# Kernel optimization log

Hardware: AMD Instinct MI355X
Metric: run time of the kernel (lower is better)

The kernel has to match this reference:

```python
import math
import jax, jax.numpy as jnp
import numpy as np

D_MODEL = 1024
NUM_HEADS = 16
HEAD_DIM = D_MODEL // NUM_HEADS
EPS = 1e-8


def setup_inputs() -> dict:
    key = jax.random.key(0)
    ks = jax.random.split(key, 9)
    B, T = 2, 2048
    scale = 1.0 / math.sqrt(D_MODEL)
    return {
        "query": jax.random.normal(ks[0], (B, T, D_MODEL), jnp.float32),
        "key": jax.random.normal(ks[1], (B, T, D_MODEL), jnp.float32),
        "value": jax.random.normal(ks[2], (B, T, D_MODEL), jnp.float32),
        "key_padding_mask": jnp.zeros((B, T), dtype=bool),
        "Wq": jax.random.normal(ks[3], (D_MODEL, D_MODEL), jnp.float32) * scale,
        "Wk": jax.random.normal(ks[4], (D_MODEL, D_MODEL), jnp.float32) * scale,
        "Wv": jax.random.normal(ks[5], (D_MODEL, D_MODEL), jnp.float32) * scale,
        "Wo": jax.random.normal(ks[6], (D_MODEL, D_MODEL), jnp.float32) * scale,
        "s_v": jnp.zeros((NUM_HEADS,), jnp.float32),
        "s_r": jnp.zeros((NUM_HEADS,), jnp.float32),
    }


def _l2norm(x, eps=EPS):
    n = jnp.sqrt(jnp.sum(x * x, axis=-1, keepdims=True))
    return x / jnp.maximum(n, eps)


def _tanh_norm(x, eps=EPS):
    # Reconstructed TanhNorm: bound each head vector by tanh of its L2 norm.
    n = jnp.sqrt(jnp.sum(x * x, axis=-1, keepdims=True))
    return jnp.tanh(n) * x / (n + eps)


def reference(query, key, value, key_padding_mask, Wq, Wk, Wv, Wo, s_v, s_r):
    B, T_q, _ = query.shape
    T_k = key.shape[1]
    H, D = NUM_HEADS, HEAD_DIM

    def proj_split(x, W):  # torch Linear: x @ W.T, then split heads -> (B,H,T,D)
        y = jnp.einsum('btm,dm->btd', x, W)
        return y.reshape(x.shape[0], x.shape[1], H, D).transpose(0, 2, 1, 3)

    q = _l2norm(proj_split(query, Wq))
    k = _l2norm(proj_split(key, Wk))
    v = _l2norm(proj_split(value, Wv))

    sim = jnp.einsum('bhqd,bhkd->bhqk', q, k)  # cosine similarities

    w = jnp.exp(s_v) + 1.0  # (H,) window size per head
    r = jnp.exp(s_r) + 1.0  # (H,) sharpness per head

    # Trim-and-Square: alpha = relu(1 - r*(1 - sim))^2
    alpha = jax.nn.relu(1.0 - r[None, :, None, None] * (1.0 - sim)) ** 2

    # Causal cosine softmask: (H, T_q, T_k)
    rel = (jnp.arange(T_k)[None, :] - jnp.arange(T_q)[:, None]).astype(jnp.float32)
    w_ = w[:, None, None]
    cos_mask = 0.5 * (jnp.cos(jnp.pi * rel[None] / w_) + 1.0)
    in_window = (rel[None] > -w_) & (rel[None] <= 0)
    softmask = cos_mask * in_window.astype(jnp.float32)
    alpha = alpha * softmask[None]

    alpha = jnp.where(key_padding_mask[:, None, None, :], 0.0, alpha)

    out = jnp.einsum('bhqk,bhkd->bhqd', alpha, v)
    out = _tanh_norm(out)
    out = out.transpose(0, 2, 1, 3).reshape(B, T_q, H * D)
    return jnp.einsum('btm,dm->btd', out, Wo)
```

## Files before the change

### kernel.cpp

```cpp
#include <hip/hip_runtime.h>
#include <math.h>

#define D_MODEL 1024
#define NUM_HEADS 16
#define HEAD_DIM 64
#define EPS 1e-8f
#define B_SZ 2
#define T_SZ 2048
#define KEXP 2048

typedef unsigned short ushort_t;
typedef __attribute__((ext_vector_type(8))) short bf16x8;
typedef __attribute__((ext_vector_type(4))) float f32x4;

__device__ __forceinline__ ushort_t f2bf(float f) {
    unsigned u = __float_as_uint(f);
    unsigned r = (u + 0x7FFFu + ((u >> 16) & 1u)) >> 16;
    return (ushort_t)r;
}
__device__ __forceinline__ float bf2f(ushort_t h) {
    return __uint_as_float(((unsigned)h) << 16);
}

__device__ __forceinline__ void gload_lds16(const ushort_t* g, ushort_t* l) {
    __builtin_amdgcn_global_load_lds(
        (const __attribute__((address_space(1))) unsigned int*)g,
        (__attribute__((address_space(3))) unsigned int*)l, 16, 0, 0);
}

__global__ __launch_bounds__(256) void expand7(
    const float* q, const float* k, const float* v,
    const float* wq, const float* wk, const float* wv, const float* wo,
    ushort_t* qe, ushort_t* ke, ushort_t* ve,
    ushort_t* wqe, ushort_t* wke, ushort_t* wve, ushort_t* woe)
{
    const float* in; ushort_t* out; int rows;
    switch (blockIdx.z) {
        case 0: in = q;  out = qe;  rows = 4096; break;
        case 1: in = k;  out = ke;  rows = 4096; break;
        case 2: in = v;  out = ve;  rows = 4096; break;
        case 3: in = wq; out = wqe; rows = 1024; break;
        case 4: in = wk; out = wke; rows = 1024; break;
        case 5: in = wv; out = wve; rows = 1024; break;
        default: in = wo; out = woe; rows = 1024; break;
    }
    const int gid = blockIdx.x * 256 + threadIdx.x;
    const int e = gid * 8;
    if (e >= rows * 1024) return;
    const int row = e >> 10;
    const int kk = e & 1023;

    float x[8];
    *(float4*)&x[0] = *(const float4*)&in[(size_t)row * 1024 + kk];
    *(float4*)&x[4] = *(const float4*)&in[(size_t)row * 1024 + kk + 4];

    union { ushort_t s[8]; uint4 u; } hi, lo;
    #pragma unroll
    for (int i = 0; i < 8; ++i) {
        ushort_t h = f2bf(x[i]);
        hi.s[i] = h;
        lo.s[i] = f2bf(x[i] - bf2f(h));
    }
    ushort_t* dst = out + (size_t)row * KEXP + (kk >> 5) * 64 + (kk & 31);
    *(uint4*)dst        = hi.u;
    *(uint4*)(dst + 32) = lo.u;
}

template<int BN, int WAVES_M, int WAVES_N>
__global__ __launch_bounds__(256) void gemm_split(
    const ushort_t* A0, const ushort_t* B0, float* C0,
    const ushort_t* A1, const ushort_t* B1, float* C1,
    const ushort_t* A2, const ushort_t* B2, float* C2,
    int M, int N)
{
    constexpr int BM = 128;
    constexpr int WAVE_M = BM / WAVES_M;
    constexpr int WAVE_N = BN / WAVES_N;
    constexpr int FM = WAVE_M / 16;
    constexpr int FN = WAVE_N / 16;
    constexpr int NLD = BM / 32 + BN / 32;

    const int gx = gridDim.x, gy = gridDim.y;
    const int nwg = gx * gy * gridDim.z;
    const int lid = blockIdx.x + gx * (blockIdx.y + gy * blockIdx.z);
    const int cpx = nwg >> 3;
    const int swz = (lid & 7) * cpx + (lid >> 3);
    const int bz  = swz / (gx * gy);
    const int rem = swz - bz * gx * gy;
    const int by  = rem / gx;
    const int bx  = rem - by * gx;

    const ushort_t* Ae; const ushort_t* Be; float* C;
    if (bz == 0)      { Ae = A0; Be = B0; C = C0; }
    else if (bz == 1) { Ae = A1; Be = B1; C = C1; }
    else              { Ae = A2; Be = B2; C = C2; }

    __shared__ __align__(16) ushort_t As0[BM * 64];
    __shared__ __align__(16) ushort_t As1[BM * 64];
    __shared__ __align__(16) ushort_t Bs0[BN * 64];
    __shared__ __align__(16) ushort_t Bs1[BN * 64];

    const int tid = threadIdx.x;
    const int bm = by * BM;
    const int bn = bx * BN;

    const int rr = tid >> 3;
    const int p  = tid & 7;

    const int wid  = tid >> 6;
    const int wm   = wid / WAVES_N;
    const int wn   = wid % WAVES_N;
    const int lane = tid & 63;
    const int lrow = lane & 15;
    const int lk   = lane >> 4;

    f32x4 acc[FM][FN] = {};

    auto stage = [&](ushort_t* AsP, ushort_t* BsP, int ks) {
        const int kb = ks * 64;
        #pragma unroll
        for (int r = 0; r < BM / 32; ++r) {
            const int row = r * 32 + rr;
            const int s = p ^ (row & 7);
            gload_lds16(Ae + (size_t)(bm + row) * KEXP + kb + s * 8,
                        &AsP[row * 64 + p * 8]);
        }
        #pragma unroll
        for (int r = 0; r < BN / 32; ++r) {
            const int row = r * 32 + rr;
            const int s = p ^ (row & 7);
            gload_lds16(Be + (size_t)(bn + row) * KEXP + kb + s * 8,
                        &BsP[row * 64 + p * 8]);
        }
    };

    auto compute = [&](const ushort_t* AsP, const ushort_t* BsP) {
        bf16x8 ah[FM], al[FM], bh[FN], bl[FN];
        #pragma unroll
        for (int m = 0; m < FM; ++m) {
            const int row = wm * WAVE_M + m * 16 + lrow;
            const int x = row & 7;
            ah[m] = *(const bf16x8*)&AsP[row * 64 + ((lk)     ^ x) * 8];
            al[m] = *(const bf16x8*)&AsP[row * 64 + ((lk + 4) ^ x) * 8];
        }
        #pragma unroll
        for (int n = 0; n < FN; ++n) {
            const int row = wn * WAVE_N + n * 16 + lrow;
            const int x = row & 7;
            bh[n] = *(const bf16x8*)&BsP[row * 64 + ((lk)     ^ x) * 8];
            bl[n] = *(const bf16x8*)&BsP[row * 64 + ((lk + 4) ^ x) * 8];
        }
        #pragma unroll
        for (int m = 0; m < FM; ++m)
            #pragma unroll
            for (int n = 0; n < FN; ++n) {
                acc[m][n] = __builtin_amdgcn_mfma_f32_16x16x32_bf16(ah[m], bh[n], acc[m][n], 0, 0, 0);
                acc[m][n] = __builtin_amdgcn_mfma_f32_16x16x32_bf16(al[m], bh[n], acc[m][n], 0, 0, 0);
                acc[m][n] = __builtin_amdgcn_mfma_f32_16x16x32_bf16(ah[m], bl[n], acc[m][n], 0, 0, 0);
            }
    };

    auto wait_nld = [&]() {
        if constexpr (NLD == 8)      asm volatile("s_waitcnt vmcnt(8)" ::: "memory");
        else if constexpr (NLD == 6) asm volatile("s_waitcnt vmcnt(6)" ::: "memory");
        else                         asm volatile("s_waitcnt vmcnt(0)" ::: "memory");
    };

    stage(As0, Bs0, 0);

    #pragma unroll 1
    for (int ks = 0; ks < 30; ks += 2) {
        stage(As1, Bs1, ks + 1);
        wait_nld();
        __builtin_amdgcn_s_barrier();
        __builtin_amdgcn_sched_barrier(0);
        compute(As0, Bs0);
        __builtin_amdgcn_s_barrier();

        stage(As0, Bs0, ks + 2);
        wait_nld();
        __builtin_amdgcn_s_barrier();
        __builtin_amdgcn_sched_barrier(0);
        compute(As1, Bs1);
        __builtin_amdgcn_s_barrier();
    }
    stage(As1, Bs1, 31);
    wait_nld();
    __builtin_amdgcn_s_barrier();
    __builtin_amdgcn_sched_barrier(0);
    compute(As0, Bs0);
    __builtin_amdgcn_s_barrier();

    asm volatile("s_waitcnt vmcnt(0)" ::: "memory");
    __builtin_amdgcn_s_barrier();
    __builtin_amdgcn_sched_barrier(0);
    compute(As1, Bs1);

    #pragma unroll
    for (int m = 0; m < FM; ++m)
        #pragma unroll
        for (int j = 0; j < 4; ++j) {
            const int row = bm + wm * WAVE_M + m * 16 + lk * 4 + j;
            float* cr = C + (size_t)row * N + bn + wn * WAVE_N + lrow;
            #pragma unroll
            for (int n = 0; n < FN; ++n)
                cr[n * 16] = acc[m][n][j];
        }
}

__device__ __forceinline__ float wred(float x) {
    #pragma unroll
    for (int off = 32; off; off >>= 1) x += __shfl_xor(x, off);
    return x;
}

__global__ __launch_bounds__(256) void attn_kernel(
    const float* __restrict__ Q, const float* __restrict__ Kp, const float* __restrict__ Vp,
    const int* __restrict__ mask, const float* __restrict__ s_v, const float* __restrict__ s_r,
    ushort_t* __restrict__ Oe)
{
    const int lane = threadIdx.x & 63;
    const int wq = (blockIdx.x * blockDim.x + threadIdx.x) >> 6;
    const int i = wq % T_SZ;
    const int h = (wq / T_SZ) % NUM_HEADS;
    const int b = wq / (T_SZ * NUM_HEADS);

    const float w = expf(s_v[h]) + 1.0f;
    const float r = expf(s_r[h]) + 1.0f;

    const size_t base = (size_t)(b * T_SZ) * D_MODEL + h * HEAD_DIM + lane;

    const float qv = Q[base + (size_t)i * D_MODEL];
    const float qn = qv / fmaxf(sqrtf(wred(qv * qv)), EPS);

    int jmin = i - (int)ceilf(w) + 1;
    if (jmin < 0) jmin = 0;

    float acc = 0.0f;
    for (int j = jmin; j <= i; ++j) {
        const float rel = (float)(j - i);
        if (!(rel > -w)) continue;
        const float kv = Kp[base + (size_t)j * D_MODEL];
        const float kn = kv / fmaxf(sqrtf(wred(kv * kv)), EPS);
        const float sim = wred(qn * kn);
        const float cm = 0.5f * (cosf((float)M_PI * rel / w) + 1.0f);
        const float a1 = fmaxf(1.0f - r * (1.0f - sim), 0.0f);
        float alpha = a1 * a1 * cm;
        if (mask[b * T_SZ + j] != 0) alpha = 0.0f;
        const float vv = Vp[base + (size_t)j * D_MODEL];
        const float vn = vv / fmaxf(sqrtf(wred(vv * vv)), EPS);
        acc += alpha * vn;
    }

    const float n = sqrtf(wred(acc * acc));
    const float o = tanhf(n) * acc / (n + EPS);

    const int row = b * T_SZ + i;
    const int kg  = h * HEAD_DIM + lane;
    ushort_t hi = f2bf(o);
    ushort_t lo = f2bf(o - bf2f(hi));
    ushort_t* dst = Oe + (size_t)row * KEXP + (kg >> 5) * 64 + (kg & 31);
    dst[0]  = hi;
    dst[32] = lo;
}

extern "C" void kernel_launch(void* const* d_in, const int* in_sizes, int n_in,
                              void* d_out, int out_size, void* d_ws, size_t ws_size,
                              hipStream_t stream) {
    const float* query = (const float*)d_in[0];
    const float* key   = (const float*)d_in[1];
    const float* value = (const float*)d_in[2];
    const int*   mask  = (const int*)d_in[3];
    const float* Wq    = (const float*)d_in[4];
    const float* Wk    = (const float*)d_in[5];
    const float* Wv    = (const float*)d_in[6];
    const float* Wo    = (const float*)d_in[7];
    const float* s_v   = (const float*)d_in[8];
    const float* s_r   = (const float*)d_in[9];
    float* out = (float*)d_out;

    const int M = B_SZ * T_SZ;
    const size_t MB = 1u << 20;

    char* ws = (char*)d_ws;
    ushort_t* qe  = (ushort_t*)(ws + 0 * MB);
    ushort_t* ke  = (ushort_t*)(ws + 16 * MB);
    ushort_t* ve  = (ushort_t*)(ws + 32 * MB);
    ushort_t* wqe = (ushort_t*)(ws + 48 * MB);
    ushort_t* wke = (ushort_t*)(ws + 52 * MB);
    ushort_t* wve = (ushort_t*)(ws + 56 * MB);
    ushort_t* woe = (ushort_t*)(ws + 60 * MB);
    float*    qp  = (float*)(ws + 64 * MB);
    float*    kp  = (float*)(ws + 80 * MB);
    float*    vp  = (float*)(ws + 96 * MB);
    ushort_t* aoe = qe;

    hipLaunchKernelGGL(expand7, dim3(2048, 1, 7), dim3(256), 0, stream,
                       query, key, value, Wq, Wk, Wv, Wo,
                       qe, ke, ve, wqe, wke, wve, woe);

    hipLaunchKernelGGL((gemm_split<128, 2, 2>), dim3(D_MODEL / 128, M / 128, 3), dim3(256), 0, stream,
                       qe, wqe, qp,
                       ke, wke, kp,
                       ve, wve, vp,
                       M, D_MODEL);

    const int total_waves = B_SZ * NUM_HEADS * T_SZ;
    hipLaunchKernelGGL(attn_kernel, dim3(total_waves / 4), dim3(256), 0, stream,
                       qp, kp, vp, mask, s_v, s_r, aoe);

    hipLaunchKernelGGL((gemm_split<64, 4, 1>), dim3(D_MODEL / 64, M / 128, 1), dim3(256), 0, stream,
                       aoe, woe, out,
                       aoe, woe, out,
                       aoe, woe, out,
                       M, D_MODEL);
}
```

Baseline: 164.0 us.

## Fuse activation bf16 hi/lo split into QKV projection GEMM

The expand kernel now converts only the four weight matrices. The Q/K/V projection GEMM reads fp32 activations directly, splits them into bf16 hi/lo parts in registers and writes them into swizzled LDS. This removes the write and re-read of the expanded activation buffers (about 48 MB of traffic). The trade-off is that the new GEMM uses single-buffered LDS with synchronous global loads of A and per-iteration conversion work, so it loses the double-buffered pipelining of the old GEMM.

```diff
diff --git a/kernel.cpp b/kernel.cpp
--- a/kernel.cpp
+++ b/kernel.cpp
@@ -28,25 +28,19 @@
         (__attribute__((address_space(3))) unsigned int*)l, 16, 0, 0);
 }
 
-__global__ __launch_bounds__(256) void expand7(
-    const float* q, const float* k, const float* v,
+__global__ __launch_bounds__(256) void expand4(
     const float* wq, const float* wk, const float* wv, const float* wo,
-    ushort_t* qe, ushort_t* ke, ushort_t* ve,
     ushort_t* wqe, ushort_t* wke, ushort_t* wve, ushort_t* woe)
 {
-    const float* in; ushort_t* out; int rows;
+    const float* in; ushort_t* out;
     switch (blockIdx.z) {
-        case 0: in = q;  out = qe;  rows = 4096; break;
-        case 1: in = k;  out = ke;  rows = 4096; break;
-        case 2: in = v;  out = ve;  rows = 4096; break;
-        case 3: in = wq; out = wqe; rows = 1024; break;
-        case 4: in = wk; out = wke; rows = 1024; break;
-        case 5: in = wv; out = wve; rows = 1024; break;
-        default: in = wo; out = woe; rows = 1024; break;
+        case 0: in = wq; out = wqe; break;
+        case 1: in = wk; out = wke; break;
+        case 2: in = wv; out = wve; break;
+        default: in = wo; out = woe; break;
     }
     const int gid = blockIdx.x * 256 + threadIdx.x;
     const int e = gid * 8;
-    if (e >= rows * 1024) return;
     const int row = e >> 10;
     const int kk = e & 1023;
 
@@ -66,19 +60,14 @@
     *(uint4*)(dst + 32) = lo.u;
 }
 
-template<int BN, int WAVES_M, int WAVES_N>
-__global__ __launch_bounds__(256) void gemm_split(
-    const ushort_t* A0, const ushort_t* B0, float* C0,
-    const ushort_t* A1, const ushort_t* B1, float* C1,
-    const ushort_t* A2, const ushort_t* B2, float* C2,
+__global__ __launch_bounds__(256) void gemm_fa(
+    const float* X0, const ushort_t* W0, float* C0,
+    const float* X1, const ushort_t* W1, float* C1,
+    const float* X2, const ushort_t* W2, float* C2,
     int M, int N)
 {
-    constexpr int BM = 128;
-    constexpr int WAVE_M = BM / WAVES_M;
-    constexpr int WAVE_N = BN / WAVES_N;
-    constexpr int FM = WAVE_M / 16;
-    constexpr int FN = WAVE_N / 16;
-    constexpr int NLD = BM / 32 + BN / 32;
+    constexpr int BM = 128, BN = 128, WAVES_N = 2;
+    constexpr int WAVE_M = 64, WAVE_N = 64, FM = 4, FN = 4;
 
     const int gx = gridDim.x, gy = gridDim.y;
     const int nwg = gx * gy * gridDim.z;
@@ -90,10 +79,132 @@
     const int by  = rem / gx;
     const int bx  = rem - by * gx;
 
-    const ushort_t* Ae; const ushort_t* Be; float* C;
-    if (bz == 0)      { Ae = A0; Be = B0; C = C0; }
-    else if (bz == 1) { Ae = A1; Be = B1; C = C1; }
-    else              { Ae = A2; Be = B2; C = C2; }
+    const float* X; const ushort_t* Be; float* C;
+    if (bz == 0)      { X = X0; Be = W0; C = C0; }
+    else if (bz == 1) { X = X1; Be = W1; C = C1; }
+    else              { X = X2; Be = W2; C = C2; }
+
+    __shared__ __align__(16) ushort_t As[BM * 64];
+    __shared__ __align__(16) ushort_t Bs[BN * 64];
+
+    const int tid = threadIdx.x;
+    const int bm = by * BM;
+    const int bn = bx * BN;
+
+    const int rr = tid >> 3;
+    const int p  = tid & 7;
+
+    const int wid  = tid >> 6;
+    const int wm   = wid / WAVES_N;
+    const int wn   = wid % WAVES_N;
+    const int lane = tid & 63;
+    const int lrow = lane & 15;
+    const int lk   = lane >> 4;
+
+    f32x4 acc[FM][FN] = {};
+
+    for (int ks = 0; ks < 32; ++ks) {
+        float4 av[4];
+        #pragma unroll
+        for (int r = 0; r < 4; ++r) {
+            const int row = r * 32 + rr;
+            av[r] = *(const float4*)&X[(size_t)(bm + row) * 1024 + ks * 32 + p * 4];
+        }
+        #pragma unroll
+        for (int r = 0; r < 4; ++r) {
+            const int row = r * 32 + rr;
+            const int s = p ^ (row & 7);
+            gload_lds16(Be + (size_t)(bn + row) * KEXP + ks * 64 + s * 8,
+                        &Bs[row * 64 + p * 8]);
+        }
+        #pragma unroll
+        for (int r = 0; r < 4; ++r) {
+            const int row = r * 32 + rr;
+            const int x7 = row & 7;
+            unsigned u0 = __float_as_uint(av[r].x) + 0x8000u;
+            unsigned u1 = __float_as_uint(av[r].y) + 0x8000u;
+            unsigned u2 = __float_as_uint(av[r].z) + 0x8000u;
+            unsigned u3 = __float_as_uint(av[r].w) + 0x8000u;
+            uint2 hiw;
+            hiw.x = (u0 >> 16) | (u1 & 0xFFFF0000u);
+            hiw.y = (u2 >> 16) | (u3 & 0xFFFF0000u);
+            float r0 = av[r].x - __uint_as_float(u0 & 0xFFFF0000u);
+            float r1 = av[r].y - __uint_as_float(u1 & 0xFFFF0000u);
+            float r2 = av[r].z - __uint_as_float(u2 & 0xFFFF0000u);
+            float r3 = av[r].w - __uint_as_float(u3 & 0xFFFF0000u);
+            unsigned v0 = __float_as_uint(r0) + 0x8000u;
+            unsigned v1 = __float_as_uint(r1) + 0x8000u;
+            unsigned v2 = __float_as_uint(r2) + 0x8000u;
+            unsigned v3 = __float_as_uint(r3) + 0x8000u;
+            uint2 low;
+            low.x = (v0 >> 16) | (v1 & 0xFFFF0000u);
+            low.y = (v2 >> 16) | (v3 & 0xFFFF0000u);
+            char* base = (char*)&As[row * 64];
+            const int bh = (((p >> 1)      ^ x7) * 16) + (p & 1) * 8;
+            const int bl = ((((p >> 1) + 4) ^ x7) * 16) + (p & 1) * 8;
+            *(uint2*)(base + bh) = hiw;
+            *(uint2*)(base + bl) = low;
+        }
+        __syncthreads();
+
+        bf16x8 ah[FM], al[FM], bh[FN], bl[FN];
+        #pragma unroll
+        for (int m = 0; m < FM; ++m) {
+            const int row = wm * WAVE_M + m * 16 + lrow;
+            const int x = row & 7;
+            ah[m] = *(const bf16x8*)&As[row * 64 + ((lk)     ^ x) * 8];
+            al[m] = *(const bf16x8*)&As[row * 64 + ((lk + 4) ^ x) * 8];
+        }
+        #pragma unroll
+        for (int n = 0; n < FN; ++n) {
+            const int row = wn * WAVE_N + n * 16 + lrow;
+            const int x = row & 7;
+            bh[n] = *(const bf16x8*)&Bs[row * 64 + ((lk)     ^ x) * 8];
+            bl[n] = *(const bf16x8*)&Bs[row * 64 + ((lk + 4) ^ x) * 8];
+        }
+        #pragma unroll
+        for (int m = 0; m < FM; ++m)
+            #pragma unroll
+            for (int n = 0; n < FN; ++n) {
+                acc[m][n] = __builtin_amdgcn_mfma_f32_16x16x32_bf16(ah[m], bh[n], acc[m][n], 0, 0, 0);
+                acc[m][n] = __builtin_amdgcn_mfma_f32_16x16x32_bf16(al[m], bh[n], acc[m][n], 0, 0, 0);
+                acc[m][n] = __builtin_amdgcn_mfma_f32_16x16x32_bf16(ah[m], bl[n], acc[m][n], 0, 0, 0);
+            }
+        __syncthreads();
+    }
+
+    #pragma unroll
+    for (int m = 0; m < FM; ++m)
+        #pragma unroll
+        for (int j = 0; j < 4; ++j) {
+            const int row = bm + wm * WAVE_M + m * 16 + lk * 4 + j;
+            float* cr = C + (size_t)row * N + bn + wn * WAVE_N + lrow;
+            #pragma unroll
+            for (int n = 0; n < FN; ++n)
+                cr[n * 16] = acc[m][n][j];
+        }
+}
+
+template<int BN, int WAVES_M, int WAVES_N>
+__global__ __launch_bounds__(256) void gemm_split(
+    const ushort_t* A0, const ushort_t* B0, float* C0, int M, int N)
+{
+    constexpr int BM = 128;
+    constexpr int WAVE_M = BM / WAVES_M;
+    constexpr int WAVE_N = BN / WAVES_N;
+    constexpr int FM = WAVE_M / 16;
+    constexpr int FN = WAVE_N / 16;
+    constexpr int NLD = BM / 32 + BN / 32;
+
+    const int gx = gridDim.x;
+    const int nwg = gx * gridDim.y;
+    const int lid = blockIdx.x + gx * blockIdx.y;
+    const int cpx = nwg >> 3;
+    const int swz = (lid & 7) * cpx + (lid >> 3);
+    const int by  = swz / gx;
+    const int bx  = swz - by * gx;
+
+    const ushort_t* Ae = A0; const ushort_t* Be = B0; float* C = C0;
 
     __shared__ __align__(16) ushort_t As0[BM * 64];
     __shared__ __align__(16) ushort_t As1[BM * 64];
@@ -283,26 +394,22 @@
     const size_t MB = 1u << 20;
 
     char* ws = (char*)d_ws;
-    ushort_t* qe  = (ushort_t*)(ws + 0 * MB);
-    ushort_t* ke  = (ushort_t*)(ws + 16 * MB);
-    ushort_t* ve  = (ushort_t*)(ws + 32 * MB);
-    ushort_t* wqe = (ushort_t*)(ws + 48 * MB);
-    ushort_t* wke = (ushort_t*)(ws + 52 * MB);
-    ushort_t* wve = (ushort_t*)(ws + 56 * MB);
-    ushort_t* woe = (ushort_t*)(ws + 60 * MB);
-    float*    qp  = (float*)(ws + 64 * MB);
-    float*    kp  = (float*)(ws + 80 * MB);
-    float*    vp  = (float*)(ws + 96 * MB);
-    ushort_t* aoe = qe;
-
-    hipLaunchKernelGGL(expand7, dim3(2048, 1, 7), dim3(256), 0, stream,
-                       query, key, value, Wq, Wk, Wv, Wo,
-                       qe, ke, ve, wqe, wke, wve, woe);
-
-    hipLaunchKernelGGL((gemm_split<128, 2, 2>), dim3(D_MODEL / 128, M / 128, 3), dim3(256), 0, stream,
-                       qe, wqe, qp,
-                       ke, wke, kp,
-                       ve, wve, vp,
+    ushort_t* wqe = (ushort_t*)(ws + 0 * MB);
+    ushort_t* wke = (ushort_t*)(ws + 4 * MB);
+    ushort_t* wve = (ushort_t*)(ws + 8 * MB);
+    ushort_t* woe = (ushort_t*)(ws + 12 * MB);
+    float*    qp  = (float*)(ws + 16 * MB);
+    float*    kp  = (float*)(ws + 32 * MB);
+    float*    vp  = (float*)(ws + 48 * MB);
+    ushort_t* aoe = (ushort_t*)(ws + 64 * MB);
+
+    hipLaunchKernelGGL(expand4, dim3(512, 1, 4), dim3(256), 0, stream,
+                       Wq, Wk, Wv, Wo, wqe, wke, wve, woe);
+
+    hipLaunchKernelGGL(gemm_fa, dim3(D_MODEL / 128, M / 128, 3), dim3(256), 0, stream,
+                       query, wqe, qp,
+                       key,   wke, kp,
+                       value, wve, vp,
                        M, D_MODEL);
 
     const int total_waves = B_SZ * NUM_HEADS * T_SZ;
@@ -310,8 +417,5 @@
                        qp, kp, vp, mask, s_v, s_r, aoe);
 
     hipLaunchKernelGGL((gemm_split<64, 4, 1>), dim3(D_MODEL / 64, M / 128, 1), dim3(256), 0, stream,
-                       aoe, woe, out,
-                       aoe, woe, out,
-                       aoe, woe, out,
-                       M, D_MODEL);
-}
+                       aoe, woe, out, M, D_MODEL);
+}
```

Measured after the change: 178.0 us. +8.5%, slower.
